# Kernel tuning notes

Hardware: AMD Instinct MI355X
Metric: run time of the kernel (lower is better)

Reference implementation:

```python
import jax, jax.numpy as jnp
import numpy as np

B, L, D, H = 4, 2048, 256, 512


def silu_backward(x):
    s = jax.nn.silu(x)
    return s + jax.nn.sigmoid(x) * (1.0 - s)


def setup_inputs() -> dict:
    key = jax.random.key(0)
    ks = jax.random.split(key, 12)
    sc = 0.02
    return {
        "x": jax.random.normal(ks[0], (B, L, D), jnp.float32),
        "W1": jax.random.normal(ks[1], (B, H, D), jnp.float32) * sc,
        "W2": jax.random.normal(ks[2], (B, D, H), jnp.float32) * sc,
        "Wq": jax.random.normal(ks[3], (D, D), jnp.float32) * sc,
        "bq": jnp.zeros((D,), jnp.float32),
        "Wk": jax.random.normal(ks[4], (D, D), jnp.float32) * sc,
        "bk": jnp.zeros((D,), jnp.float32),
        "Wv": jax.random.normal(ks[5], (D, D), jnp.float32) * sc,
        "bv": jnp.zeros((D,), jnp.float32),
        "w_lr": jax.random.normal(ks[6], (D,), jnp.float32) * sc,
        "b_lr": jnp.zeros((), jnp.float32),
        "w_wd": jax.random.normal(ks[7], (D,), jnp.float32) * sc,
        "b_wd": jnp.zeros((), jnp.float32),
        "log_base_lr": jnp.asarray(np.log(0.1), jnp.float32),
        "log_base_wd": jnp.asarray(np.log(0.5), jnp.float32),
    }


def reference(x, W1, W2, Wq, bq, Wk, bk, Wv, bv, w_lr, b_lr, w_wd, b_wd, log_base_lr, log_base_wd):
    b, l, d = x.shape
    query = x @ Wq + bq
    key = x @ Wk + bk
    value = x @ Wv + bv
    lr = jnp.exp(log_base_lr) * jax.nn.sigmoid(x @ w_lr + b_lr)          # [b,l]
    log_wd = jnp.log(1.0 - jnp.exp(log_base_wd) * jax.nn.sigmoid(x @ w_wd + b_wd))  # [b,l]

    wd_cross = jnp.exp(jnp.cumsum(log_wd, axis=1))                       # [b,l]
    idx = jnp.arange(l)
    strict_upper = idx[:, None] < idx[None, :]                           # (m, j): j > m
    A = jnp.where(strict_upper[None], log_wd[:, None, :], 0.0)           # [b,m,j]
    wd_inner = jnp.exp(jnp.cumsum(A, axis=2)) * (idx[:, None] <= idx[None, :])[None]  # [b,m,j]

    X1 = key
    Z1 = jnp.einsum('bhd,bld->blh', W1, X1)
    X2 = jax.nn.silu(Z1)
    Z2 = jnp.einsum('bdh,blh->bld', W2, X2)
    grad_Z2 = Z2 - value
    grad_X2 = jnp.einsum('bdh,bld->blh', W2, grad_Z2)
    grad_Z1 = silu_backward(Z1) * grad_X2

    X1_ = query
    mask_X1X1_ = jnp.einsum('bld,bmd->blm', X1, X1_) * wd_inner
    Z1_inner = -jnp.einsum('blh,bl,blm->bmh', grad_Z1, lr, mask_X1X1_)
    Z1_cross = jnp.einsum('bhd,bld,bl->blh', W1, X1_, wd_cross)
    Z1_ = Z1_inner + Z1_cross

    W1_next = (-jnp.einsum('blh,bl,bld->bhd', grad_Z1, lr * wd_inner[:, :, -1], X1)
               + W1 * wd_cross[:, -1][:, None, None])

    X2_ = jax.nn.silu(Z1_)
    mask_X2X2_ = jnp.einsum('blh,bmh->blm', X2, X2_) * wd_inner
    Z2_inner = -jnp.einsum('bld,bl,blm->bmd', grad_Z2, lr, mask_X2X2_)
    Z2_cross = jnp.einsum('bdh,blh,bl->bld', W2, X2_, wd_cross)
    Z2_ = Z2_inner + Z2_cross

    W2_next = (-jnp.einsum('bld,bl,blh->bdh', grad_Z2, lr * wd_inner[:, :, -1], X2)
               + W2 * wd_cross[:, -1][:, None, None])

    return (Z2_, W1_next, W2_next)
```

## Files before the change

kernel.cpp:

```cpp
#include <hip/hip_runtime.h>

typedef __bf16 bf16;
typedef __bf16 bf16x8 __attribute__((ext_vector_type(8)));
typedef __bf16 bf16x4 __attribute__((ext_vector_type(4)));
typedef float  f32x4  __attribute__((ext_vector_type(4)));

#define SB 72
#define CUTOFF -18.0

__device__ __forceinline__ float silu_f(float x){
  float s = 1.f/(1.f+__expf(-x));
  return x*s;
}
__device__ __forceinline__ float silu_bwd_f(float x){
  float s = 1.f/(1.f+__expf(-x));
  float si = x*s;
  return si + s*(1.f-si);
}

struct MArgs {
  const bf16* A; const bf16* B;
  long sA, sB;
  int lda, ldb;
  int M, N, K;
  int mode;
  float* Cf; long sCf;
  bf16*  Cb; long sCb;
  bf16*  Cb2; long sCb2;
  bf16*  Ct;  long sCt;  int ldct;
  bf16*  Ct2; long sCt2;
  int ldc;
  const float* auxf; int ldax; long sAuxf;
  const bf16*  auxb; long sAuxb;
  const float* rowv; long sRowv;
  const float* rowv2; long sRowv2;
  const double* cd;  long sCd;
  const float* clp;  long sClp;
  bf16* Q; bf16* Ko; float* Vo; const float* bqkv;
};

template<int TM>
__device__ __forceinline__ void gemm_body(const MArgs& g, int bm, int bn, int bz)
{
  constexpr int TTP = (TM==64) ? 72 : 136;
  __shared__ __align__(16) bf16 sh[(TM+64)*SB];
  bf16* As = sh;
  bf16* Bs = sh + TM*SB;

  const int row0 = bm*TM, col0 = bn*64;
  constexpr int NI  = TM/32;
  constexpr int TPR = 256/TM;
  constexpr int EPR = 64/TPR;
  constexpr int NCH = EPR/8;

  const bf16* A = g.A + (long)bz*g.sA;
  const bf16* B = g.B + (long)bz*g.sB;
  const double* cd = g.cd ? g.cd + (long)bz*g.sCd : (const double*)0;
  float* Cf = g.Cf ? g.Cf + (long)bz*g.sCf : (float*)0;
  bf16* Cb  = g.Cb ? g.Cb + (long)bz*g.sCb : (bf16*)0;
  bf16* Cb2 = g.Cb2 ? g.Cb2 + (long)bz*g.sCb2 : (bf16*)0;
  bf16* Ct  = g.Ct ? g.Ct + (long)bz*g.sCt : (bf16*)0;
  bf16* Ct2 = g.Ct2 ? g.Ct2 + (long)bz*g.sCt2 : (bf16*)0;
  const float* auxf = g.auxf ? g.auxf + (long)bz*g.sAuxf : (const float*)0;
  const bf16*  auxb = g.auxb ? g.auxb + (long)bz*g.sAuxb : (const bf16*)0;
  const float* rowv = g.rowv ? g.rowv + (long)bz*g.sRowv : (const float*)0;
  const float* rowv2 = g.rowv2 ? g.rowv2 + (long)bz*g.sRowv2 : (const float*)0;

  const int tid = threadIdx.x;
  const int mode = g.mode;
  const int lane = tid & 63;
  const int w = tid >> 6;
  const int wr = (w >> 1) * (TM/2), wc = (w & 1) * 32;
  const int l15 = lane & 15;
  const int quad = lane >> 4;

  f32x4 acc[NI][2];
  #pragma unroll
  for (int i=0;i<NI;i++)
    #pragma unroll
    for (int j=0;j<2;j++)
      #pragma unroll
      for (int r=0;r<4;r++) acc[i][j][r] = 0.f;

  const int rowA = tid / TPR, kA = (tid % TPR) * EPR;
  const int rowB = tid >> 2,  kB = (tid & 3) * 16;

  int klo = 0;
  if (cd) {
    const double cref = cd[g.K-1];
    const int nch = g.K >> 6;
    bool dead = (lane < nch-1) && ((cref - cd[lane*64+63]) < CUTOFF);
    unsigned long long mask = __ballot(dead);
    klo = (int)__builtin_ctzll(~mask) * 64;
  }

  const bf16* Abase = A + (long)(row0+rowA)*g.lda + kA;
  const bf16* Bbase = B + (long)(col0+rowB)*g.ldb + kB;

  bf16x8 pa[NCH], pb[2];
  #pragma unroll
  for (int p=0;p<NCH;p++) pa[p] = *(const bf16x8*)(Abase + klo + p*8);
  pb[0] = *(const bf16x8*)(Bbase + klo);
  pb[1] = *(const bf16x8*)(Bbase + klo + 8);

  for (int k0 = klo; k0 < g.K; k0 += 64) {
    #pragma unroll
    for (int p=0;p<NCH;p++) *(bf16x8*)&As[rowA*SB + kA + p*8] = pa[p];
    *(bf16x8*)&Bs[rowB*SB + kB]     = pb[0];
    *(bf16x8*)&Bs[rowB*SB + kB + 8] = pb[1];
    __syncthreads();
    const bool more = (k0 + 64) < g.K;
    bf16x8 na[NCH], nb[2];
    if (more) {
      #pragma unroll
      for (int p=0;p<NCH;p++) na[p] = *(const bf16x8*)(Abase + k0 + 64 + p*8);
      nb[0] = *(const bf16x8*)(Bbase + k0 + 64);
      nb[1] = *(const bf16x8*)(Bbase + k0 + 64 + 8);
    }
    #pragma unroll
    for (int ch=0; ch<2; ch++){
      bf16x8 af[NI], bf2[2];
      #pragma unroll
      for (int i=0;i<NI;i++) af[i]  = *(const bf16x8*)&As[(wr + i*16 + l15)*SB + ch*32 + quad*8];
      #pragma unroll
      for (int j=0;j<2;j++) bf2[j] = *(const bf16x8*)&Bs[(wc + j*16 + l15)*SB + ch*32 + quad*8];
      #pragma unroll
      for (int i=0;i<NI;i++)
        #pragma unroll
        for (int j=0;j<2;j++)
          acc[i][j] = __builtin_amdgcn_mfma_f32_16x16x32_bf16(af[i], bf2[j], acc[i][j], 0, 0, 0);
    }
    __syncthreads();
    if (more) {
      #pragma unroll
      for (int p=0;p<NCH;p++) pa[p] = na[p];
      pb[0] = nb[0]; pb[1] = nb[1];
    }
  }

  float clv = 0.f;
  if (mode == 10) clv = *(g.clp + (long)bz*g.sClp);

  const bool hasT = (TM==64) ? (mode==1 || mode==2 || mode==3)
                             : (mode==11 && col0 >= 256 && col0 < 512);

  #pragma unroll
  for (int i=0;i<NI;i++){
    const int rb = row0 + wr + i*16 + quad*4;
    const int rloc = wr + i*16 + quad*4;
    #pragma unroll
    for (int j=0;j<2;j++){
      const int c = col0 + wc + j*16 + l15;
      const int cloc = wc + j*16 + l15;
      bf16 tv[4], tv2[4]; bool doT = false, doT2 = false;
      #pragma unroll
      for (int reg=0; reg<4; reg++){
        const int r = rb + reg;
        float v = acc[i][j][reg];
        const long co = (long)r*g.ldc + c;
        switch (mode) {
          case 1: {
            Cb[co]  = (bf16)v;
            float sv = silu_f(v);
            Cb2[co] = (bf16)sv;
            tv[reg] = (bf16)(sv * rowv[r]); doT = true;
          } break;
          case 2: {
            bf16 o = (bf16)(v - auxf[(long)r*g.ldax + c]);
            Cb[co] = o; tv[reg] = o; doT = true;
          } break;
          case 3: {
            float v3 = silu_bwd_f((float)auxb[(long)r*g.ldax + c]) * v * rowv[r];
            tv[reg]  = (bf16)v3;
            tv2[reg] = (bf16)(v3 * rowv2[r]);
            doT = true; doT2 = true;
          } break;
          case 10: {
            Cf[co] = v + auxf[(long)r*g.ldax + c]*clv;
          } break;
          case 11: {
            float o = v + g.bqkv[c];
            if (c < 256)      g.Q [(long)r*256 + c]       = (bf16)o;
            else if (c < 512) { g.Ko[(long)r*256 + (c-256)] = (bf16)o; tv[reg] = (bf16)o; doT = true; }
            else              g.Vo[(long)r*256 + (c-512)] = o;
          } break;
        }
      }
      if (hasT && doT) {
        bf16x4 t4 = { tv[0], tv[1], tv[2], tv[3] };
        *(bf16x4*)&sh[cloc*TTP + rloc] = t4;
        if (doT2) {
          bf16x4 t4b = { tv2[0], tv2[1], tv2[2], tv2[3] };
          *(bf16x4*)&sh[64*72 + cloc*TTP + rloc] = t4b;
        }
      }
    }
  }

  if (hasT) {
    __syncthreads();
    if constexpr (TM == 64) {
      const int cl = tid >> 2, rl = (tid & 3)*16;
      bf16x8 u0 = *(const bf16x8*)&sh[cl*72 + rl];
      bf16x8 u1 = *(const bf16x8*)&sh[cl*72 + rl + 8];
      bf16* d = Ct + (long)(col0+cl)*g.ldct + row0 + rl;
      *(bf16x8*)d       = u0;
      *(bf16x8*)(d + 8) = u1;
      if (mode == 3) {
        bf16x8 v0 = *(const bf16x8*)&sh[64*72 + cl*72 + rl];
        bf16x8 v1 = *(const bf16x8*)&sh[64*72 + cl*72 + rl + 8];
        bf16* d2 = Ct2 + (long)(col0+cl)*g.ldct + row0 + rl;
        *(bf16x8*)d2       = v0;
        *(bf16x8*)(d2 + 8) = v1;
      }
    } else {
      const int cl = tid >> 2, rl = (tid & 3)*32;
      const int b = row0 / g.ldct, l0r = row0 % g.ldct;
      bf16* d = Ct + (long)b*g.sCt + (long)(col0-256+cl)*g.ldct + l0r + rl;
      #pragma unroll
      for (int p=0;p<4;p++)
        *(bf16x8*)(d + p*8) = *(const bf16x8*)&sh[cl*136 + rl + p*8];
    }
  }
}

__global__ __launch_bounds__(256)
void mfma_gemm128(MArgs g){ gemm_body<128>(g, blockIdx.x, blockIdx.y, blockIdx.z); }

__global__ __launch_bounds__(256)
void mfma_gemm64(MArgs g){ gemm_body<64>(g, blockIdx.x, blockIdx.y, blockIdx.z); }

__global__ __launch_bounds__(256)
void wnext_gemm(MArgs g1, MArgs g2){
  const int z = blockIdx.z;
  const MArgs& g = (z < 4) ? g1 : g2;
  const int bz = z & 3;
  if ((int)blockIdx.x*128 >= g.M || (int)blockIdx.y*64 >= g.N) return;
  gemm_body<128>(g, blockIdx.x, blockIdx.y, bz);
}

struct PArgs {
  const bf16 *A, *B1;
  long sA, sB1;
  const double* cd; long sCd;
  const float* lrv; long sLr;
  bf16* P;
};

template<int KS64, int ISLR>
__global__ __launch_bounds__(256)
void pgen(PArgs g)
{
  const int mt = blockIdx.x, slot = blockIdx.y, bz = blockIdx.z;
  const int m0 = mt*64;
  const int l0 = (m0 & ~127) - slot*128;
  if (l0 < 0) return;
  const double* cd = g.cd + (long)bz*g.sCd;
  const int lref = (l0+127 < m0) ? (l0+127) : m0;
  if (cd[m0] - cd[lref] < CUTOFF) return;

  const int K1 = KS64*64;
  const bf16* A  = g.A  + (long)bz*g.sA;
  const bf16* B1 = g.B1 + (long)bz*g.sB1;
  const float* lrv = ISLR ? (g.lrv + (long)bz*g.sLr) : (const float*)0;

  const int tid = threadIdx.x;
  const int lane = tid & 63, w = tid >> 6;
  const int wr = (w>>1)*32, wc = (w&1)*64;
  const int l15 = lane & 15, quad = lane >> 4;
  const int rowA = tid >> 2, kA = (tid & 3) * 16;
  const int rowB = tid >> 1, kB = (tid & 1) * 32;

  __shared__ __align__(16) bf16 As[64*SB];
  __shared__ __align__(16) bf16 Bs[128*SB];

  f32x4 O[2][4];
  #pragma unroll
  for (int i=0;i<2;i++)
    #pragma unroll
    for (int j=0;j<4;j++)
      #pragma unroll
      for (int r=0;r<4;r++) O[i][j][r] = 0.f;

  const bf16* Abase = A + (long)(m0+rowA)*K1 + kA;
  const bf16* Bbase = B1 + (long)(l0+rowB)*K1 + kB;

  bf16x8 pa[2], pb[4];
  pa[0] = *(const bf16x8*)Abase;
  pa[1] = *(const bf16x8*)(Abase + 8);
  #pragma unroll
  for (int p=0;p<4;p++) pb[p] = *(const bf16x8*)(Bbase + p*8);

  for (int ks=0; ks<KS64; ks++){
    const int k0 = ks*64;
    *(bf16x8*)&As[rowA*SB + kA]     = pa[0];
    *(bf16x8*)&As[rowA*SB + kA + 8] = pa[1];
    #pragma unroll
    for (int p=0;p<4;p++) *(bf16x8*)&Bs[rowB*SB + kB + p*8] = pb[p];
    __syncthreads();
    const bool more = (ks+1) < KS64;
    bf16x8 na[2], nb[4];
    if (more) {
      na[0] = *(const bf16x8*)(Abase + k0 + 64);
      na[1] = *(const bf16x8*)(Abase + k0 + 64 + 8);
      #pragma unroll
      for (int p=0;p<4;p++) nb[p] = *(const bf16x8*)(Bbase + k0 + 64 + p*8);
    }
    #pragma unroll
    for (int ch=0; ch<2; ch++){
      bf16x8 af[2], bfr[4];
      #pragma unroll
      for (int i=0;i<2;i++) af[i]  = *(const bf16x8*)&As[(wr + i*16 + l15)*SB + ch*32 + quad*8];
      #pragma unroll
      for (int j=0;j<4;j++) bfr[j] = *(const bf16x8*)&Bs[(wc + j*16 + l15)*SB + ch*32 + quad*8];
      #pragma unroll
      for (int i=0;i<2;i++)
        #pragma unroll
        for (int j=0;j<4;j++)
          O[i][j] = __builtin_amdgcn_mfma_f32_16x16x32_bf16(af[i], bfr[j], O[i][j], 0, 0, 0);
    }
    __syncthreads();
    if (more) {
      pa[0] = na[0]; pa[1] = na[1];
      #pragma unroll
      for (int p=0;p<4;p++) pb[p] = nb[p];
    }
  }

  bf16* Pt = g.P + (((long)bz*32 + mt)*3 + slot) * (64*128);
  float cl[4], lv[4];
  #pragma unroll
  for (int j=0;j<4;j++){
    const int l = l0 + wc + j*16 + l15;
    cl[j] = (float)cd[l];
    if (ISLR) lv[j] = lrv[l];
  }
  #pragma unroll
  for (int i=0;i<2;i++)
    #pragma unroll
    for (int reg=0; reg<4; reg++){
      const int mloc = wr + i*16 + quad*4 + reg;
      const int m = m0 + mloc;
      const float cm = (float)cd[m];
      #pragma unroll
      for (int j=0;j<4;j++){
        const int lloc = wc + j*16 + l15;
        const int l = l0 + lloc;
        float v = -O[i][j][reg] * __expf(cm - cl[j]);
        if (ISLR) v *= lv[j];
        if (l > m) v = 0.f;
        Pt[mloc*128 + lloc] = (bf16)v;
      }
    }
}

struct CArgs {
  const bf16 *A, *W, *P, *B2;
  long sA, sW, sB2;
  int ldb2;
  const double* cd; long sCd;
  const float* wdc; long sWdc;
  float* Cf; long sCf;
  bf16* Cb; long sCb;
  int ldc;
};

template<int KS64, int SILU, int ZSPLIT>
__global__ __launch_bounds__(256)
void cons(CArgs g)
{
  const int mt = blockIdx.x;
  const int m0 = mt*64, n0 = blockIdx.y*64;
  const int bz   = ZSPLIT ? (blockIdx.z >> 1) : blockIdx.z;
  const int half = ZSPLIT ? (blockIdx.z & 1)  : 0;
  const int K1 = KS64*64;
  const bf16* A  = g.A  + (long)bz*g.sA;
  const bf16* W  = g.W  + (long)bz*g.sW;
  const bf16* B2 = g.B2 + (long)bz*g.sB2;
  const double* cd = g.cd + (long)bz*g.sCd;
  const float* wdc = g.wdc + (long)bz*g.sWdc;

  const int tid = threadIdx.x;
  const int lane = tid & 63, w = tid >> 6;
  const int wr = (w>>1)*32, wc = (w&1)*32;
  const int l15 = lane & 15, quad = lane >> 4;
  const int rowA = tid >> 2, kA = (tid & 3) * 16;

  bool alive[3];
  int nalive = 0;
  #pragma unroll
  for (int s=0;s<3;s++){
    const int l0 = (m0 & ~127) - s*128;
    bool a = (l0 >= 0);
    if (a) {
      const int lref = (l0+127 < m0) ? (l0+127) : m0;
      a = (cd[m0] - cd[lref] >= CUTOFF);
    }
    alive[s] = a; nalive += a ? 1 : 0;
  }
  if (ZSPLIT && half == 1 && nalive == 0) return;

  __shared__ __align__(16) bf16 As[64*SB];
  __shared__ __align__(16) bf16 Bs[64*SB];

  f32x4 O[2][2];
  #pragma unroll
  for (int i=0;i<2;i++)
    #pragma unroll
    for (int j=0;j<2;j++)
      #pragma unroll
      for (int r=0;r<4;r++) O[i][j][r] = 0.f;

  if (half == 0) {
    const bf16* Abase = A + (long)(m0+rowA)*K1 + kA;
    const bf16* Wbase = W + (long)(n0+rowA)*K1 + kA;
    bf16x8 pa[2], pw[2];
    pa[0] = *(const bf16x8*)Abase;      pa[1] = *(const bf16x8*)(Abase + 8);
    pw[0] = *(const bf16x8*)Wbase;      pw[1] = *(const bf16x8*)(Wbase + 8);
    for (int ks=0; ks<KS64; ks++){
      const int k0 = ks*64;
      *(bf16x8*)&As[rowA*SB + kA]     = pa[0];
      *(bf16x8*)&As[rowA*SB + kA + 8] = pa[1];
      *(bf16x8*)&Bs[rowA*SB + kA]     = pw[0];
      *(bf16x8*)&Bs[rowA*SB + kA + 8] = pw[1];
      __syncthreads();
      const bool more = (ks+1) < KS64;
      bf16x8 na[2], nw[2];
      if (more) {
        na[0] = *(const bf16x8*)(Abase + k0 + 64);
        na[1] = *(const bf16x8*)(Abase + k0 + 64 + 8);
        nw[0] = *(const bf16x8*)(Wbase + k0 + 64);
        nw[1] = *(const bf16x8*)(Wbase + k0 + 64 + 8);
      }
      #pragma unroll
      for (int ch=0; ch<2; ch++){
        bf16x8 af[2], bfr[2];
        #pragma unroll
        for (int i=0;i<2;i++) af[i]  = *(const bf16x8*)&As[(wr + i*16 + l15)*SB + ch*32 + quad*8];
        #pragma unroll
        for (int j=0;j<2;j++) bfr[j] = *(const bf16x8*)&Bs[(wc + j*16 + l15)*SB + ch*32 + quad*8];
        #pragma unroll
        for (int i=0;i<2;i++)
          #pragma unroll
          for (int j=0;j<2;j++)
            O[i][j] = __builtin_amdgcn_mfma_f32_16x16x32_bf16(af[i], bfr[j], O[i][j], 0, 0, 0);
      }
      __syncthreads();
      if (more) { pa[0]=na[0]; pa[1]=na[1]; pw[0]=nw[0]; pw[1]=nw[1]; }
    }
    #pragma unroll
    for (int i=0;i<2;i++)
      #pragma unroll
      for (int reg=0; reg<4; reg++){
        const float s = wdc[m0 + wr + i*16 + quad*4 + reg];
        #pragma unroll
        for (int j=0;j<2;j++) O[i][j][reg] *= s;
      }
  }

  if (!ZSPLIT || half == 1) {
    for (int s=0; s<3; s++){
      if (!alive[s]) continue;
      const int l0 = (m0 & ~127) - s*128;
      const bf16* Pt = g.P + (((long)bz*32 + mt)*3 + s) * (64*128);
      const bf16* Pb = Pt + (long)rowA*128 + kA;
      const bf16* Bb = B2 + (long)(n0+rowA)*g.ldb2 + l0 + kA;
      bf16x8 rp0 = *(const bf16x8*)Pb,  rp1 = *(const bf16x8*)(Pb+8);
      bf16x8 rb0 = *(const bf16x8*)Bb,  rb1 = *(const bf16x8*)(Bb+8);
      #pragma unroll
      for (int hk=0; hk<2; hk++){
        *(bf16x8*)&As[rowA*SB + kA]     = rp0;
        *(bf16x8*)&As[rowA*SB + kA + 8] = rp1;
        *(bf16x8*)&Bs[rowA*SB + kA]     = rb0;
        *(bf16x8*)&Bs[rowA*SB + kA + 8] = rb1;
        __syncthreads();
        if (hk == 0) {
          rp0 = *(const bf16x8*)(Pb + 64); rp1 = *(const bf16x8*)(Pb + 72);
          rb0 = *(const bf16x8*)(Bb + 64); rb1 = *(const bf16x8*)(Bb + 72);
        }
        #pragma unroll
        for (int ch=0; ch<2; ch++){
          bf16x8 af[2], bfr[2];
          #pragma unroll
          for (int i=0;i<2;i++) af[i]  = *(const bf16x8*)&As[(wr + i*16 + l15)*SB + ch*32 + quad*8];
          #pragma unroll
          for (int j=0;j<2;j++) bfr[j] = *(const bf16x8*)&Bs[(wc + j*16 + l15)*SB + ch*32 + quad*8];
          #pragma unroll
          for (int i=0;i<2;i++)
            #pragma unroll
            for (int j=0;j<2;j++)
              O[i][j] = __builtin_amdgcn_mfma_f32_16x16x32_bf16(af[i], bfr[j], O[i][j], 0, 0, 0);
        }
        __syncthreads();
      }
    }
  }

  #pragma unroll
  for (int i=0;i<2;i++){
    const int rb = m0 + wr + i*16 + quad*4;
    #pragma unroll
    for (int j=0;j<2;j++){
      const int c = n0 + wc + j*16 + l15;
      #pragma unroll
      for (int reg=0; reg<4; reg++){
        const long co = (long)(rb+reg)*g.ldc + c;
        if (ZSPLIT)     unsafeAtomicAdd(&g.Cf[(long)bz*g.sCf + co], O[i][j][reg]);
        else if (SILU)  g.Cb[(long)bz*g.sCb + co] = (bf16)silu_f(O[i][j][reg]);
        else            g.Cf[(long)bz*g.sCf + co] = O[i][j][reg];
      }
    }
  }
}

struct FrontArgs {
  const float *x, *W1, *W2, *Wq, *Wk, *Wv;
  bf16 *xb, *W1b, *W2b, *Wqkvt, *W2t;
  float* out0;
  const float *wlr, *blr, *wwd, *bwd, *lbl, *lbw;
  float *lr, *lw;
  long LD4, HD4, HD;
};

__global__ __launch_bounds__(256)
void front_kernel(FrontArgs f)
{
  __shared__ bf16 t[64][72];
  const int bid = blockIdx.x;
  const int tid = threadIdx.x;

  if (bid < 1536) {
    const float* src; bf16* dst; long n; long base;
    if (bid < 1024)      { src = f.x;  dst = f.xb;  n = f.LD4; base = (long)bid*2048; }
    else if (bid < 1280) { src = f.W1; dst = f.W1b; n = f.HD4; base = (long)(bid-1024)*2048; }
    else                 { src = f.W2; dst = f.W2b; n = f.HD4; base = (long)(bid-1280)*2048; }
    long i = base + (long)tid*8;
    if (i >= n) return;
    float4 a = *(const float4*)&src[i];
    float4 b = *(const float4*)&src[i+4];
    bf16x8 o;
    o[0]=(bf16)a.x; o[1]=(bf16)a.y; o[2]=(bf16)a.z; o[3]=(bf16)a.w;
    o[4]=(bf16)b.x; o[5]=(bf16)b.y; o[6]=(bf16)b.z; o[7]=(bf16)b.w;
    *(bf16x8*)&dst[i] = o;
    return;
  }
  if (bid < 2560) {
    long i = (long)(bid-1536)*2048 + (long)tid*8;
    float4 z = {0.f,0.f,0.f,0.f};
    *(float4*)&f.out0[i]   = z;
    *(float4*)&f.out0[i+4] = z;
    return;
  }
  if (bid < 2736) {
    const float* ip; bf16* op; int R, C; int r0, c0;
    if (bid < 2608) {
      const int r = bid - 2560;
      const int z = r >> 4, rem = r & 15;
      ip = z==0 ? f.Wq : (z==1 ? f.Wk : f.Wv);
      op = f.Wqkvt + (long)z*256*256;
      R = 256; C = 256;
      r0 = (rem & 3)*64; c0 = (rem >> 2)*64;
    } else {
      const int r = bid - 2608;
      const int b = r >> 5, rem = r & 31;
      ip = f.W2 + (long)b*f.HD;
      op = f.W2t + (long)b*f.HD;
      R = 256; C = 512;
      r0 = (rem & 3)*64; c0 = (rem >> 2)*64;
    }
    const int lr_ = tid>>2, lc = (tid&3)*16;
    #pragma unroll
    for (int q=0;q<4;q++){
      float4 a = *(const float4*)&ip[(long)(r0+lr_)*C + c0+lc + q*4];
      t[lr_][lc+q*4+0] = (bf16)a.x; t[lr_][lc+q*4+1] = (bf16)a.y;
      t[lr_][lc+q*4+2] = (bf16)a.z; t[lr_][lc+q*4+3] = (bf16)a.w;
    }
    __syncthreads();
    const int oc = tid>>2, orr = (tid&3)*16;
    bf16x8 u, v;
    #pragma unroll
    for (int i=0;i<8;i++){ u[i] = t[orr+i][oc]; v[i] = t[orr+8+i][oc]; }
    *(bf16x8*)&op[(long)(c0+oc)*R + r0+orr]   = u;
    *(bf16x8*)&op[(long)(c0+oc)*R + r0+orr+8] = v;
    return;
  }
  {
    const int row  = (bid-2736)*4 + (tid >> 6);
    const int lane = tid & 63;
    const float4 a = ((const float4*)(f.x + (long)row*256))[lane];
    const float4 u = ((const float4*)f.wlr)[lane];
    const float4 w = ((const float4*)f.wwd)[lane];
    float d1 = a.x*u.x + a.y*u.y + a.z*u.z + a.w*u.w;
    float d2 = a.x*w.x + a.y*w.y + a.z*w.z + a.w*w.w;
    #pragma unroll
    for (int off=32; off; off>>=1) {
      d1 += __shfl_down(d1, off);
      d2 += __shfl_down(d2, off);
    }
    if (lane == 0) {
      float s1 = 1.f/(1.f+expf(-(d1 + f.blr[0])));
      f.lr[row] = expf(f.lbl[0]) * s1;
      float s2 = 1.f/(1.f+expf(-(d2 + f.bwd[0])));
      f.lw[row] = logf(1.f - expf(f.lbw[0]) * s2);
    }
  }
}

__global__ __launch_bounds__(256)
void cumsum_kernel(const float* __restrict__ lw, const float* __restrict__ lr,
                   double* __restrict__ cd, float* __restrict__ wdc,
                   float* __restrict__ se1, float* __restrict__ se2, int L,
                   const float* __restrict__ bq, const float* __restrict__ bk,
                   const float* __restrict__ bv, float* __restrict__ bqkv)
{
  const int b = blockIdx.x;
  const int t = threadIdx.x;
  if (b == 4) {
    for (int i = t; i < 768; i += 256)
      bqkv[i] = (i<256) ? bq[i] : ((i<512) ? bk[i-256] : bv[i-512]);
    return;
  }
  const float* lwb = lw + (long)b*L;
  __shared__ double sum_s[256];
  double loc[8];
  double s = 0.0;
  #pragma unroll
  for (int i=0;i<8;i++){ s += (double)lwb[t*8+i]; loc[i] = s; }
  sum_s[t] = s;
  __syncthreads();
  for (int off=1; off<256; off<<=1){
    double v = 0.0;
    if (t >= off) v = sum_s[t-off];
    __syncthreads();
    sum_s[t] += v;
    __syncthreads();
  }
  const double prefix = (t > 0) ? sum_s[t-1] : 0.0;
  const double total  = sum_s[255];
  #pragma unroll
  for (int i=0;i<8;i++){
    double c = prefix + loc[i];
    long idx = (long)b*L + t*8 + i;
    cd[idx]  = c;
    wdc[idx] = (float)exp(c);
    double e = exp(total - c);
    se1[idx] = (float)(-e);
    se2[idx] = (float)(-e) * lr[idx];
  }
}

extern "C" void kernel_launch(void* const* d_in, const int* in_sizes, int n_in,
                              void* d_out, int out_size, void* d_ws, size_t ws_size,
                              hipStream_t stream)
{
  const int Bn = 4, L = 2048, D = 256, H = 512;
  const long LD = (long)L*D, LH = (long)L*H, HD = (long)H*D;

  const float* x   = (const float*)d_in[0];
  const float* W1  = (const float*)d_in[1];
  const float* W2  = (const float*)d_in[2];
  const float* Wq  = (const float*)d_in[3];
  const float* bq  = (const float*)d_in[4];
  const float* Wk  = (const float*)d_in[5];
  const float* bk  = (const float*)d_in[6];
  const float* Wv  = (const float*)d_in[7];
  const float* bv  = (const float*)d_in[8];
  const float* wlr = (const float*)d_in[9];
  const float* blr = (const float*)d_in[10];
  const float* wwd = (const float*)d_in[11];
  const float* bwd = (const float*)d_in[12];
  const float* lbl = (const float*)d_in[13];
  const float* lbw = (const float*)d_in[14];
  (void)in_sizes; (void)n_in; (void)out_size; (void)ws_size;

  float* out0 = (float*)d_out;
  float* out1 = out0 + (long)Bn*LD;
  float* out2 = out1 + (long)Bn*HD;

  char* wsp = (char*)d_ws;
  size_t off = 0;
  auto alloc = [&](size_t bytes)->void*{
    void* p = wsp + off; off += (bytes + 255) & ~(size_t)255; return p;
  };
  bf16* xb    = (bf16*)alloc((size_t)Bn*LD*2);
  bf16* Wqkvt = (bf16*)alloc((size_t)3*D*D*2);
  float* bqkv = (float*)alloc((size_t)3*D*4);
  bf16* W1b  = (bf16*)alloc((size_t)Bn*HD*2);
  bf16* W2b  = (bf16*)alloc((size_t)Bn*HD*2);
  bf16* W2t  = (bf16*)alloc((size_t)Bn*HD*2);
  bf16* Qb   = (bf16*)alloc((size_t)Bn*LD*2);
  bf16* Kb   = (bf16*)alloc((size_t)Bn*LD*2);
  bf16* Kt   = (bf16*)alloc((size_t)Bn*LD*2);
  float* Vf  = (float*)alloc((size_t)Bn*LD*4);
  bf16* Z1b  = (bf16*)alloc((size_t)Bn*LH*2);
  bf16* X2b  = (bf16*)alloc((size_t)Bn*LH*2);
  bf16* X2t  = (bf16*)alloc((size_t)Bn*LH*2);
  bf16* gZb  = (bf16*)alloc((size_t)Bn*LD*2);
  bf16* gZt  = (bf16*)alloc((size_t)Bn*LD*2);
  bf16* A1t  = (bf16*)alloc((size_t)Bn*LH*2);
  bf16* A1s  = (bf16*)alloc((size_t)Bn*LH*2);
  bf16* X2_b = (bf16*)alloc((size_t)Bn*LH*2);
  bf16* Pb1  = (bf16*)alloc((size_t)Bn*32*3*64*128*2);
  bf16* Pb2  = (bf16*)alloc((size_t)Bn*32*3*64*128*2);
  float* lrb = (float*)alloc((size_t)Bn*L*4);
  float* lwb = (float*)alloc((size_t)Bn*L*4);
  float* wdc = (float*)alloc((size_t)Bn*L*4);
  float* se1 = (float*)alloc((size_t)Bn*L*4);
  float* se2 = (float*)alloc((size_t)Bn*L*4);
  double* cdb = (double*)alloc((size_t)Bn*L*8);

  auto run128 = [&](const MArgs& g, int Z){
    dim3 grid(g.M/128, g.N/64, Z);
    mfma_gemm128<<<grid, 256, 0, stream>>>(g);
  };
  auto run64 = [&](const MArgs& g, int Z){
    dim3 grid(g.M/64, g.N/64, Z);
    mfma_gemm64<<<grid, 256, 0, stream>>>(g);
  };

  {
    FrontArgs f{};
    f.x = x; f.W1 = W1; f.W2 = W2; f.Wq = Wq; f.Wk = Wk; f.Wv = Wv;
    f.xb = xb; f.W1b = W1b; f.W2b = W2b; f.Wqkvt = Wqkvt; f.W2t = W2t;
    f.out0 = out0;
    f.wlr = wlr; f.blr = blr; f.wwd = wwd; f.bwd = bwd; f.lbl = lbl; f.lbw = lbw;
    f.lr = lrb; f.lw = lwb;
    f.LD4 = Bn*LD; f.HD4 = Bn*HD; f.HD = HD;
    front_kernel<<<dim3(4784), 256, 0, stream>>>(f);
  }
  cumsum_kernel<<<dim3(5), 256, 0, stream>>>(lwb, lrb, cdb, wdc, se1, se2, L, bq, bk, bv, bqkv);

  {
    MArgs g{}; g.A = xb; g.lda = D; g.B = Wqkvt; g.ldb = D;
    g.M = Bn*L; g.N = 3*D; g.K = D; g.mode = 11; g.ldc = 0;
    g.Q = Qb; g.Ko = Kb; g.Vo = Vf; g.bqkv = bqkv;
    g.Ct = Kt; g.sCt = LD; g.ldct = L;
    run128(g, 1);
  }
  {
    MArgs g{}; g.A = Kb; g.lda = D; g.sA = LD; g.B = W1b; g.ldb = D; g.sB = HD;
    g.M = L; g.N = H; g.K = D; g.mode = 1; g.ldc = H;
    g.Cb = Z1b; g.sCb = LH; g.Cb2 = X2b; g.sCb2 = LH;
    g.Ct = X2t; g.sCt = LH; g.ldct = L;
    g.rowv = se2; g.sRowv = L;
    run64(g, Bn);
  }
  {
    MArgs g{}; g.A = X2b; g.lda = H; g.sA = LH; g.B = W2b; g.ldb = H; g.sB = HD;
    g.M = L; g.N = D; g.K = H; g.mode = 2; g.ldc = D;
    g.auxf = Vf; g.ldax = D; g.sAuxf = LD; g.Cb = gZb; g.sCb = LD;
    g.Ct = gZt; g.sCt = LD; g.ldct = L; run64(g, Bn);
  }
  {
    MArgs g{}; g.A = gZb; g.lda = D; g.sA = LD; g.B = W2t; g.ldb = D; g.sB = HD;
    g.M = L; g.N = H; g.K = D; g.mode = 3; g.ldc = H;
    g.auxb = Z1b; g.ldax = H; g.sAuxb = LH;
    g.rowv = lrb; g.sRowv = L; g.rowv2 = se1; g.sRowv2 = L;
    g.Ct = A1t; g.sCt = LH; g.ldct = L;
    g.Ct2 = A1s; g.sCt2 = LH;
    run64(g, Bn);
  }
  {
    PArgs p{};
    p.A = Qb; p.sA = LD; p.B1 = Kb; p.sB1 = LD;
    p.cd = cdb; p.sCd = L; p.P = Pb1;
    pgen<4,0><<<dim3(32,3,Bn), 256, 0, stream>>>(p);
  }
  {
    CArgs c{};
    c.A = Qb; c.sA = LD; c.W = W1b; c.sW = HD;
    c.P = Pb1; c.B2 = A1t; c.sB2 = LH; c.ldb2 = L;
    c.cd = cdb; c.sCd = L; c.wdc = wdc; c.sWdc = L;
    c.Cb = X2_b; c.sCb = LH; c.ldc = H;
    cons<4,1,0><<<dim3(32, H/64, Bn), 256, 0, stream>>>(c);
  }
  {
    PArgs p{};
    p.A = X2_b; p.sA = LH; p.B1 = X2b; p.sB1 = LH;
    p.cd = cdb; p.sCd = L; p.lrv = lrb; p.sLr = L; p.P = Pb2;
    pgen<8,1><<<dim3(32,3,Bn), 256, 0, stream>>>(p);
  }
  {
    CArgs c{};
    c.A = X2_b; c.sA = LH; c.W = W2b; c.sW = HD;
    c.P = Pb2; c.B2 = gZt; c.sB2 = LD; c.ldb2 = L;
    c.cd = cdb; c.sCd = L; c.wdc = wdc; c.sWdc = L;
    c.Cf = out0; c.sCf = LD; c.ldc = D;
    cons<8,0,1><<<dim3(32, D/64, Bn*2), 256, 0, stream>>>(c);
  }
  {
    MArgs g1{}; g1.A = A1s; g1.lda = L; g1.sA = LH; g1.B = Kt; g1.ldb = L; g1.sB = LD;
    g1.M = H; g1.N = D; g1.K = L; g1.mode = 10; g1.ldc = D;
    g1.cd = cdb; g1.sCd = L;
    g1.auxf = W1; g1.ldax = D; g1.sAuxf = HD; g1.clp = wdc + (L-1); g1.sClp = L;
    g1.Cf = out1; g1.sCf = HD;

    MArgs g2{}; g2.A = gZt; g2.lda = L; g2.sA = LD; g2.B = X2t; g2.ldb = L; g2.sB = LH;
    g2.M = D; g2.N = H; g2.K = L; g2.mode = 10; g2.ldc = H;
    g2.cd = cdb; g2.sCd = L;
    g2.auxf = W2; g2.ldax = H; g2.sAuxf = HD; g2.clp = wdc + (L-1); g2.sClp = L;
    g2.Cf = out2; g2.sCf = HD;

    wnext_gemm<<<dim3(4,8,8), 256, 0, stream>>>(g1, g2);
  }
}
```

Measured before the change: 223.8 us.

## Double-buffer LDS tiles to drop trailing barrier; use 64-row tiles for W-next GEMM

The gemm_body, pgen and cons kernels now use two shared-memory buffers that alternate each k-step. This removes the second __syncthreads per iteration and the register copy of the prefetched tiles, so the next global loads are issued straight into the staging registers. Separately, the W-next GEMM switches from 128-row to 64-row tiles with twice as many blocks to raise parallelism. The cost is double the LDS footprint per block, which can lower occupancy. The epilogues that reuse the shared array for transposes may also need to be checked for races now that the final barrier is gone.

```diff
diff --git a/kernel.cpp b/kernel.cpp
--- a/kernel.cpp
+++ b/kernel.cpp
@@ -43,9 +43,8 @@
 __device__ __forceinline__ void gemm_body(const MArgs& g, int bm, int bn, int bz)
 {
   constexpr int TTP = (TM==64) ? 72 : 136;
-  __shared__ __align__(16) bf16 sh[(TM+64)*SB];
-  bf16* As = sh;
-  bf16* Bs = sh + TM*SB;
+  constexpr int BUF = (TM+64)*SB;
+  __shared__ __align__(16) bf16 sh[2*BUF];
 
   const int row0 = bm*TM, col0 = bn*64;
   constexpr int NI  = TM/32;
@@ -103,19 +102,21 @@
   pb[0] = *(const bf16x8*)(Bbase + klo);
   pb[1] = *(const bf16x8*)(Bbase + klo + 8);
 
+  int cur = 0;
   for (int k0 = klo; k0 < g.K; k0 += 64) {
+    bf16* As = sh + cur*BUF;
+    bf16* Bs = As + TM*SB;
     #pragma unroll
     for (int p=0;p<NCH;p++) *(bf16x8*)&As[rowA*SB + kA + p*8] = pa[p];
     *(bf16x8*)&Bs[rowB*SB + kB]     = pb[0];
     *(bf16x8*)&Bs[rowB*SB + kB + 8] = pb[1];
     __syncthreads();
     const bool more = (k0 + 64) < g.K;
-    bf16x8 na[NCH], nb[2];
     if (more) {
       #pragma unroll
-      for (int p=0;p<NCH;p++) na[p] = *(const bf16x8*)(Abase + k0 + 64 + p*8);
-      nb[0] = *(const bf16x8*)(Bbase + k0 + 64);
-      nb[1] = *(const bf16x8*)(Bbase + k0 + 64 + 8);
+      for (int p=0;p<NCH;p++) pa[p] = *(const bf16x8*)(Abase + k0 + 64 + p*8);
+      pb[0] = *(const bf16x8*)(Bbase + k0 + 64);
+      pb[1] = *(const bf16x8*)(Bbase + k0 + 64 + 8);
     }
     #pragma unroll
     for (int ch=0; ch<2; ch++){
@@ -130,12 +131,7 @@
         for (int j=0;j<2;j++)
           acc[i][j] = __builtin_amdgcn_mfma_f32_16x16x32_bf16(af[i], bf2[j], acc[i][j], 0, 0, 0);
     }
-    __syncthreads();
-    if (more) {
-      #pragma unroll
-      for (int p=0;p<NCH;p++) pa[p] = na[p];
-      pb[0] = nb[0]; pb[1] = nb[1];
-    }
+    cur ^= 1;
   }
 
   float clv = 0.f;
@@ -235,8 +231,8 @@
   const int z = blockIdx.z;
   const MArgs& g = (z < 4) ? g1 : g2;
   const int bz = z & 3;
-  if ((int)blockIdx.x*128 >= g.M || (int)blockIdx.y*64 >= g.N) return;
-  gemm_body<128>(g, blockIdx.x, blockIdx.y, bz);
+  if ((int)blockIdx.x*64 >= g.M || (int)blockIdx.y*64 >= g.N) return;
+  gemm_body<64>(g, blockIdx.x, blockIdx.y, bz);
 }
 
 struct PArgs {
@@ -271,8 +267,8 @@
   const int rowA = tid >> 2, kA = (tid & 3) * 16;
   const int rowB = tid >> 1, kB = (tid & 1) * 32;
 
-  __shared__ __align__(16) bf16 As[64*SB];
-  __shared__ __align__(16) bf16 Bs[128*SB];
+  constexpr int BUFP = (64+128)*SB;
+  __shared__ __align__(16) bf16 sh[2*BUFP];
 
   f32x4 O[2][4];
   #pragma unroll
@@ -291,20 +287,22 @@
   #pragma unroll
   for (int p=0;p<4;p++) pb[p] = *(const bf16x8*)(Bbase + p*8);
 
+  int cur = 0;
   for (int ks=0; ks<KS64; ks++){
     const int k0 = ks*64;
+    bf16* As = sh + cur*BUFP;
+    bf16* Bs = As + 64*SB;
     *(bf16x8*)&As[rowA*SB + kA]     = pa[0];
     *(bf16x8*)&As[rowA*SB + kA + 8] = pa[1];
     #pragma unroll
     for (int p=0;p<4;p++) *(bf16x8*)&Bs[rowB*SB + kB + p*8] = pb[p];
     __syncthreads();
     const bool more = (ks+1) < KS64;
-    bf16x8 na[2], nb[4];
     if (more) {
-      na[0] = *(const bf16x8*)(Abase + k0 + 64);
-      na[1] = *(const bf16x8*)(Abase + k0 + 64 + 8);
-      #pragma unroll
-      for (int p=0;p<4;p++) nb[p] = *(const bf16x8*)(Bbase + k0 + 64 + p*8);
+      pa[0] = *(const bf16x8*)(Abase + k0 + 64);
+      pa[1] = *(const bf16x8*)(Abase + k0 + 64 + 8);
+      #pragma unroll
+      for (int p=0;p<4;p++) pb[p] = *(const bf16x8*)(Bbase + k0 + 64 + p*8);
     }
     #pragma unroll
     for (int ch=0; ch<2; ch++){
@@ -319,12 +317,7 @@
         for (int j=0;j<4;j++)
           O[i][j] = __builtin_amdgcn_mfma_f32_16x16x32_bf16(af[i], bfr[j], O[i][j], 0, 0, 0);
     }
-    __syncthreads();
-    if (more) {
-      pa[0] = na[0]; pa[1] = na[1];
-      #pragma unroll
-      for (int p=0;p<4;p++) pb[p] = nb[p];
-    }
+    cur ^= 1;
   }
 
   bf16* Pt = g.P + (((long)bz*32 + mt)*3 + slot) * (64*128);
@@ -400,8 +393,8 @@
   }
   if (ZSPLIT && half == 1 && nalive == 0) return;
 
-  __shared__ __align__(16) bf16 As[64*SB];
-  __shared__ __align__(16) bf16 Bs[64*SB];
+  constexpr int BUFC = 128*SB;
+  __shared__ __align__(16) bf16 sh[2*BUFC];
 
   f32x4 O[2][2];
   #pragma unroll
@@ -410,6 +403,8 @@
     for (int j=0;j<2;j++)
       #pragma unroll
       for (int r=0;r<4;r++) O[i][j][r] = 0.f;
+
+  int cur = 0;
 
   if (half == 0) {
     const bf16* Abase = A + (long)(m0+rowA)*K1 + kA;
@@ -419,18 +414,19 @@
     pw[0] = *(const bf16x8*)Wbase;      pw[1] = *(const bf16x8*)(Wbase + 8);
     for (int ks=0; ks<KS64; ks++){
       const int k0 = ks*64;
+      bf16* As = sh + cur*BUFC;
+      bf16* Bs = As + 64*SB;
       *(bf16x8*)&As[rowA*SB + kA]     = pa[0];
       *(bf16x8*)&As[rowA*SB + kA + 8] = pa[1];
       *(bf16x8*)&Bs[rowA*SB + kA]     = pw[0];
       *(bf16x8*)&Bs[rowA*SB + kA + 8] = pw[1];
       __syncthreads();
       const bool more = (ks+1) < KS64;
-      bf16x8 na[2], nw[2];
       if (more) {
-        na[0] = *(const bf16x8*)(Abase + k0 + 64);
-        na[1] = *(const bf16x8*)(Abase + k0 + 64 + 8);
-        nw[0] = *(const bf16x8*)(Wbase + k0 + 64);
-        nw[1] = *(const bf16x8*)(Wbase + k0 + 64 + 8);
+        pa[0] = *(const bf16x8*)(Abase + k0 + 64);
+        pa[1] = *(const bf16x8*)(Abase + k0 + 64 + 8);
+        pw[0] = *(const bf16x8*)(Wbase + k0 + 64);
+        pw[1] = *(const bf16x8*)(Wbase + k0 + 64 + 8);
       }
       #pragma unroll
       for (int ch=0; ch<2; ch++){
@@ -445,8 +441,7 @@
           for (int j=0;j<2;j++)
             O[i][j] = __builtin_amdgcn_mfma_f32_16x16x32_bf16(af[i], bfr[j], O[i][j], 0, 0, 0);
       }
-      __syncthreads();
-      if (more) { pa[0]=na[0]; pa[1]=na[1]; pw[0]=nw[0]; pw[1]=nw[1]; }
+      cur ^= 1;
     }
     #pragma unroll
     for (int i=0;i<2;i++)
@@ -469,6 +464,8 @@
       bf16x8 rb0 = *(const bf16x8*)Bb,  rb1 = *(const bf16x8*)(Bb+8);
       #pragma unroll
       for (int hk=0; hk<2; hk++){
+        bf16* As = sh + cur*BUFC;
+        bf16* Bs = As + 64*SB;
         *(bf16x8*)&As[rowA*SB + kA]     = rp0;
         *(bf16x8*)&As[rowA*SB + kA + 8] = rp1;
         *(bf16x8*)&Bs[rowA*SB + kA]     = rb0;
@@ -491,7 +488,7 @@
             for (int j=0;j<2;j++)
               O[i][j] = __builtin_amdgcn_mfma_f32_16x16x32_bf16(af[i], bfr[j], O[i][j], 0, 0, 0);
         }
-        __syncthreads();
+        cur ^= 1;
       }
     }
   }
@@ -801,6 +798,6 @@
     g2.auxf = W2; g2.ldax = H; g2.sAuxf = HD; g2.clp = wdc + (L-1); g2.sClp = L;
     g2.Cf = out2; g2.sCf = HD;
 
-    wnext_gemm<<<dim3(4,8,8), 256, 0, stream>>>(g1, g2);
+    wnext_gemm<<<dim3(8,8,8), 256, 0, stream>>>(g1, g2);
   }
 }
```

Result: no change. 224.6 us (+0.4%).
